# Kernel optimization log

Measured on AMD Instinct MI355X. Metric: run time of the kernel, lower is better.

Reference implementation:

```python
import jax, jax.numpy as jnp
import numpy as np

B, N, K = 32, 1024, 20

def _knn_idx(x, k):
    # x: [B, N, C] -> indices of k nearest neighbors (excluding self): [B, N, k]
    sq = jnp.sum(x * x, axis=-1)                      # [B, N]
    d = sq[:, :, None] + sq[:, None, :] - 2.0 * jnp.einsum('bnc,bmc->bnm', x, x)
    d = jnp.where(jnp.eye(x.shape[1], dtype=bool)[None], jnp.inf, d)
    _, idx = jax.lax.top_k(-d, k)                     # smallest distances
    return idx

def _edge_conv(x, k, mlp):
    # x: [B, N, C]; dynamic kNN graph + nn(cat[x_i, x_j - x_i]) + max over neighbors
    idx = _knn_idx(x, k)                              # [B, N, k]
    xj = jax.vmap(lambda xb, ib: xb[ib])(x, idx)      # [B, N, k, C]
    xi = jnp.broadcast_to(x[:, :, None, :], xj.shape)
    msg = mlp(jnp.concatenate([xi, xj - xi], axis=-1))  # [B, N, k, H]
    return jnp.max(msg, axis=2)                       # [B, N, H]

def setup_inputs() -> dict:
    key = jax.random.key(0)
    ks = jax.random.split(key, 16)
    def lin(kk, fi, fo):
        return jax.random.normal(kk, (fi, fo), dtype=jnp.float32) / np.sqrt(fi)
    x = jax.random.normal(ks[0], (B * N, 3), dtype=jnp.float32)
    batch = jnp.repeat(jnp.arange(B, dtype=jnp.int64), N)
    return {
        'x': x, 'batch': batch,
        'W1': lin(ks[1], 6, 64),   'b1': jnp.zeros((64,), jnp.float32),
        'W2': lin(ks[2], 64, 64),  'b2': jnp.zeros((64,), jnp.float32),
        'W3': lin(ks[3], 64, 64),  'b3': jnp.zeros((64,), jnp.float32),
        'W4': lin(ks[4], 128, 128),'b4': jnp.zeros((128,), jnp.float32),
        'Wp': lin(ks[5], 128, 512),'bp': jnp.zeros((512,), jnp.float32),
        'Wt1': lin(ks[6], 512, 256),'bt1': jnp.zeros((256,), jnp.float32),
        'Wt2': lin(ks[7], 256, 40), 'bt2': jnp.zeros((40,), jnp.float32),
    }

def reference(x, batch, W1, b1, W2, b2, W3, b3, W4, b4, Wp, bp, Wt1, bt1, Wt2, bt2):
    xb = x.reshape(B, N, -1)  # equal-sized clouds per batch vector
    mlp1 = lambda h: jax.nn.relu(jax.nn.relu(jax.nn.relu(h @ W1 + b1) @ W2 + b2) @ W3 + b3)
    mlp2 = lambda h: jax.nn.relu(h @ W4 + b4)
    out = _edge_conv(xb, K, mlp1)          # [B, N, 64]
    out = _edge_conv(out, K, mlp2)         # [B, N, 128]
    out = jax.nn.relu(out @ Wp + bp)       # [B, N, 512]
    out = jnp.max(out, axis=1)             # global max pool -> [B, 512]
    out = jax.nn.relu(out @ Wt1 + bt1) @ Wt2 + bt2  # [B, 40]
    return out
```

## Files before the change

### kernel.cpp

```cpp
#include <hip/hip_runtime.h>
#include <math.h>

#define BN   1024
#define NB   32
#define KNN  20
#define NROWS (NB*BN)

typedef __attribute__((ext_vector_type(8))) short bf16x8_t;
typedef __attribute__((ext_vector_type(4))) float f32x4_t;

__device__ __forceinline__ float finf() { return __builtin_huge_valf(); }

__device__ __forceinline__ unsigned short f2bf(float f) {
  union { float f; unsigned u; } v; v.f = f;
  unsigned r = v.u + 0x7FFFu + ((v.u >> 16) & 1u);
  return (unsigned short)(r >> 16);
}
__device__ __forceinline__ float bf2f(unsigned short h) {
  union { unsigned u; float f; } v; v.u = ((unsigned)h) << 16; return v.f;
}

__device__ __forceinline__ unsigned fkey(float d) {
  union { float f; unsigned u; } v; v.f = d;
  return (v.u & 0x80000000u) ? ~v.u : (v.u | 0x80000000u);
}

__device__ __forceinline__ void emit20(const unsigned (&kq)[16], unsigned thr,
                                       int lane, unsigned short* __restrict__ idx_out) {
  const unsigned long long lmask = (1ull << lane) - 1ull;
  int base = 0;
#pragma unroll
  for (int t = 0; t < 16; ++t) {
    const bool ok = (kq[t] <= thr);
    const unsigned long long m = __ballot(ok);
    if (ok) idx_out[base + (int)__popcll(m & lmask)] = (unsigned short)(kq[t] & 1023u);
    base += (int)__popcll(m);
  }
}

__device__ __forceinline__ void emit20c(const unsigned (&kq)[16], unsigned P, int cnt_lt,
                                        int lane, unsigned short* __restrict__ idx_out) {
  const unsigned long long lmask = (1ull << lane) - 1ull;
  const int need = KNN - cnt_lt;
  int base_lt = 0, base_eq = 0;
#pragma unroll
  for (int t = 0; t < 16; ++t) {
    const bool lt = (kq[t] < P);
    const bool eq = ((kq[t] - P) < 1024u);
    const unsigned long long mlt = __ballot(lt);
    const unsigned long long meq = __ballot(eq);
    if (lt) idx_out[base_lt + (int)__popcll(mlt & lmask)] = (unsigned short)(kq[t] & 1023u);
    const int erank = base_eq + (int)__popcll(meq & lmask);
    if (eq && erank < need) idx_out[cnt_lt + erank] = (unsigned short)(kq[t] & 1023u);
    base_lt += (int)__popcll(mlt);
    base_eq += (int)__popcll(meq);
  }
}

__device__ __forceinline__ void select20x2(const unsigned (&k0)[16], const unsigned (&k1)[16],
    int lane, unsigned short* __restrict__ o0, unsigned short* __restrict__ o1) {
  unsigned p0 = 0u, p1 = 0u;
  bool d0 = false, d1 = false;
#pragma unroll 1
  for (int b = 31; b >= 10; --b) {
    if (!d0) {
      const unsigned cand = p0 | (1u << b);
      int cnt = 0;
#pragma unroll
      for (int t = 0; t < 16; ++t) cnt += (int)__popcll(__ballot(k0[t] < cand));
      if (cnt == KNN)      { p0 = cand - 1u; d0 = true; }
      else if (cnt < KNN)  { p0 = cand; }
    }
    if (!d1) {
      const unsigned cand = p1 | (1u << b);
      int cnt = 0;
#pragma unroll
      for (int t = 0; t < 16; ++t) cnt += (int)__popcll(__ballot(k1[t] < cand));
      if (cnt == KNN)      { p1 = cand - 1u; d1 = true; }
      else if (cnt < KNN)  { p1 = cand; }
    }
    if (d0 && d1) break;
  }
  if (d0) emit20(k0, p0, lane, o0);
  else {
    int c = 0;
#pragma unroll
    for (int t = 0; t < 16; ++t) c += (int)__popcll(__ballot(k0[t] < p0));
    emit20c(k0, p0, c, lane, o0);
  }
  if (d1) emit20(k1, p1, lane, o1);
  else {
    int c = 0;
#pragma unroll
    for (int t = 0; t < 16; ++t) c += (int)__popcll(__ballot(k1[t] < p1));
    emit20c(k1, p1, c, lane, o1);
  }
}

__global__ __launch_bounds__(256) void prep_kernel(const float* __restrict__ W2, const float* __restrict__ W3,
    const float* __restrict__ W4, const float* __restrict__ Wp,
    unsigned short* __restrict__ w2b, unsigned short* __restrict__ w3b,
    unsigned short* __restrict__ w4b, unsigned short* __restrict__ wpb) {
  const int i = blockIdx.x * 256 + threadIdx.x;
  if (i < 512) {
    const int lane = i & 63, ks = (i >> 6) & 1, nt = i >> 7;
    const int col = nt*16 + (lane & 15), k0 = ks*32 + ((lane >> 4) << 3);
#pragma unroll
    for (int e = 0; e < 8; ++e) w2b[i*8 + e] = f2bf(W2[(size_t)(k0 + e)*64 + col]);
  } else if (i < 1024) {
    const int ii = i - 512;
    const int lane = ii & 63, ks = (ii >> 6) & 1, nt = ii >> 7;
    const int col = nt*16 + (lane & 15), k0 = ks*32 + ((lane >> 4) << 3);
#pragma unroll
    for (int e = 0; e < 8; ++e) w3b[ii*8 + e] = f2bf(W3[(size_t)(k0 + e)*64 + col]);
  } else if (i < 3072) {
    const int ii = i - 1024;
    const int lane = ii & 63, ks = (ii >> 6) & 3, nt = ii >> 8;
    const int col = nt*16 + (lane & 15), k0 = ks*32 + ((lane >> 4) << 3);
#pragma unroll
    for (int e = 0; e < 8; ++e) w4b[ii*8 + e] = f2bf(W4[(size_t)(k0 + e)*128 + col]);
  } else if (i < 11264) {
    const int ii = i - 3072;
    const int lane = ii & 63, ks = (ii >> 6) & 3, nt = ii >> 8;
    const int col = nt*16 + (lane & 15), k0 = ks*32 + ((lane >> 4) << 3);
#pragma unroll
    for (int e = 0; e < 8; ++e) {
      const float v = Wp[(size_t)(k0 + e)*512 + col];
      const unsigned short h = f2bf(v);
      wpb[ii*8 + e]         = h;
      wpb[65536 + ii*8 + e] = f2bf(v - bf2f(h));
    }
  }
}

__global__ __launch_bounds__(256) void knn3_kernel(const float* __restrict__ x, unsigned short* __restrict__ idxo) {
  const int pair = blockIdx.x * 4 + (threadIdx.x >> 6);
  const int lane = threadIdx.x & 63;
  const int row0 = pair * 2;
  const int b = row0 >> 10;
  const int ia = row0 & (BN - 1), ib = ia + 1;
  const float* xb = x + (size_t)b * BN * 3;
  const float xa0 = xb[ia*3+0], xa1 = xb[ia*3+1], xa2 = xb[ia*3+2];
  const float xb0 = xb[ib*3+0], xb1 = xb[ib*3+1], xb2 = xb[ib*3+2];
  const float sqa = xa0*xa0 + xa1*xa1 + xa2*xa2;
  const float sqb = xb0*xb0 + xb1*xb1 + xb2*xb2;
  unsigned k0[16], k1[16];
#pragma unroll
  for (int t = 0; t < 16; ++t) {
    const int j = (t << 6) | lane;
    const float a0 = xb[j*3+0], a1 = xb[j*3+1], a2 = xb[j*3+2];
    const float sqj = a0*a0 + a1*a1 + a2*a2;
    const float da  = sqa + sqj - 2.0f*(xa0*a0 + xa1*a1 + xa2*a2);
    const float db  = sqb + sqj - 2.0f*(xb0*a0 + xb1*a1 + xb2*a2);
    k0[t] = (j == ia) ? 0xFFFFFFFFu : ((fkey(da) & 0xFFFFFC00u) | (unsigned)j);
    k1[t] = (j == ib) ? 0xFFFFFFFFu : ((fkey(db) & 0xFFFFFC00u) | (unsigned)j);
  }
  select20x2(k0, k1, lane, idxo + (size_t)row0 * KNN, idxo + (size_t)(row0 + 1) * KNN);
}

__global__ __launch_bounds__(256) void edge1_mfma_kernel(const float* __restrict__ x, const unsigned short* __restrict__ idx,
    const float* __restrict__ W1, const float* __restrict__ B1,
    const unsigned short* __restrict__ w2b, const float* __restrict__ B2,
    const unsigned short* __restrict__ w3b, const float* __restrict__ B3,
    unsigned short* __restrict__ hib, unsigned short* __restrict__ lob,
    float* __restrict__ sqbuf) {
  __shared__ unsigned short Hs1[80*64];
  __shared__ unsigned short Hs2[80*64];
  __shared__ float part[4][4];
  const int t = threadIdx.x, lane = t & 63, w = t >> 6;
  const int node0 = blockIdx.x * 4;

  const int bcol = w*16 + (lane & 15);
  bf16x8_t Bf2[2], Bf3[2];
#pragma unroll
  for (int ks = 0; ks < 2; ++ks) {
    Bf2[ks] = *(const bf16x8_t*)&w2b[(size_t)((w*2 + ks)*64 + lane) * 8];
    Bf3[ks] = *(const bf16x8_t*)&w3b[(size_t)((w*2 + ks)*64 + lane) * 8];
  }

  float w1c[6];
#pragma unroll
  for (int c = 0; c < 6; ++c) w1c[c] = W1[c*64 + lane];
  const float b1o = B1[lane];
  for (int r = w; r < 80; r += 4) {
    const int g = (r * 205) >> 12;
    const int e = r - g*20;
    const int node = node0 + g;
    const int b = node >> 10;
    const int j = idx[(size_t)node*KNN + e];
    const float xi0 = x[(size_t)node*3+0], xi1 = x[(size_t)node*3+1], xi2 = x[(size_t)node*3+2];
    const size_t jr = ((size_t)(b*BN + j))*3;
    const float h3 = x[jr+0]-xi0, h4 = x[jr+1]-xi1, h5 = x[jr+2]-xi2;
    float z = b1o + xi0*w1c[0] + xi1*w1c[1] + xi2*w1c[2]
                  + h3*w1c[3] + h4*w1c[4] + h5*w1c[5];
    z = fmaxf(z, 0.0f);
    Hs1[r*64 + (((lane>>3) ^ (r&7))<<3) + (lane&7)] = f2bf(z);
  }
  __syncthreads();

  f32x4_t acc[5];
#pragma unroll
  for (int mt = 0; mt < 5; ++mt) acc[mt] = (f32x4_t){0,0,0,0};
#pragma unroll
  for (int ks = 0; ks < 2; ++ks) {
#pragma unroll
    for (int mt = 0; mt < 5; ++mt) {
      const int r = mt*16 + (lane & 15);
      const int chunk = ks*4 + (lane >> 4);
      const bf16x8_t a = *(const bf16x8_t*)&Hs1[r*64 + ((chunk ^ (r&7))<<3)];
      acc[mt] = __builtin_amdgcn_mfma_f32_16x16x32_bf16(a, Bf2[ks], acc[mt], 0,0,0);
    }
  }
  {
    const float b2o = B2[bcol];
    const int rbase = (lane >> 4) * 4;
#pragma unroll
    for (int mt = 0; mt < 5; ++mt) {
#pragma unroll
      for (int reg = 0; reg < 4; ++reg) {
        const int row = mt*16 + rbase + reg;
        const float v = fmaxf(acc[mt][reg] + b2o, 0.0f);
        Hs2[row*64 + (((bcol>>3) ^ (row&7))<<3) + (bcol&7)] = f2bf(v);
      }
    }
  }
  __syncthreads();

#pragma unroll
  for (int mt = 0; mt < 5; ++mt) acc[mt] = (f32x4_t){0,0,0,0};
#pragma unroll
  for (int ks = 0; ks < 2; ++ks) {
#pragma unroll
    for (int mt = 0; mt < 5; ++mt) {
      const int r = mt*16 + (lane & 15);
      const int chunk = ks*4 + (lane >> 4);
      const bf16x8_t a = *(const bf16x8_t*)&Hs2[r*64 + ((chunk ^ (r&7))<<3)];
      acc[mt] = __builtin_amdgcn_mfma_f32_16x16x32_bf16(a, Bf3[ks], acc[mt], 0,0,0);
    }
  }

  {
    const float b3o = B3[bcol];
    const int rbase = (lane >> 4) * 4;
    float nm0 = 0.0f, nm1 = 0.0f, nm2 = 0.0f, nm3 = 0.0f;
#pragma unroll
    for (int mt = 0; mt < 5; ++mt) {
#pragma unroll
      for (int reg = 0; reg < 4; ++reg) {
        const int r = mt*16 + rbase + reg;
        const int g = (r * 205) >> 12;
        const float v = fmaxf(acc[mt][reg] + b3o, 0.0f);
        nm0 = (g == 0) ? fmaxf(nm0, v) : nm0;
        nm1 = (g == 1) ? fmaxf(nm1, v) : nm1;
        nm2 = (g == 2) ? fmaxf(nm2, v) : nm2;
        nm3 = (g == 3) ? fmaxf(nm3, v) : nm3;
      }
    }
#pragma unroll
    for (int off = 16; off <= 32; off <<= 1) {
      nm0 = fmaxf(nm0, __shfl_xor(nm0, off, 64));
      nm1 = fmaxf(nm1, __shfl_xor(nm1, off, 64));
      nm2 = fmaxf(nm2, __shfl_xor(nm2, off, 64));
      nm3 = fmaxf(nm3, __shfl_xor(nm3, off, 64));
    }
    const int gq = lane >> 4;
    const float m = (gq == 0) ? nm0 : (gq == 1) ? nm1 : (gq == 2) ? nm2 : nm3;
    const int node = node0 + gq;
    const unsigned short h = f2bf(m);
    hib[(size_t)node*64 + bcol] = h;
    lob[(size_t)node*64 + bcol] = f2bf(m - bf2f(h));
    float s = m * m;
#pragma unroll
    for (int off = 1; off <= 8; off <<= 1) s += __shfl_xor(s, off, 64);
    if ((lane & 15) == 0) part[gq][w] = s;
  }
  __syncthreads();
  if (t < 4) sqbuf[node0 + t] = part[t][0] + part[t][1] + part[t][2] + part[t][3];
}

__global__ __launch_bounds__(512) void knn64edge2_kernel(
    const unsigned short* __restrict__ hi, const unsigned short* __restrict__ lo,
    const float* __restrict__ sq, const unsigned short* __restrict__ w4b,
    const float* __restrict__ B4,
    unsigned short* __restrict__ o2hi, unsigned short* __restrict__ o2lo) {
  __shared__ unsigned Dmat[16 * 1024];
  __shared__ unsigned short idx_sh[16][KNN];
  unsigned short* Hs = (unsigned short*)Dmat;
  const int t = threadIdx.x, lane = t & 63, w = t >> 6;
  const int i0  = blockIdx.x * 16;
  const int b   = i0 >> 10;
  const int i0l = i0 & (BN - 1);

  {
    const size_t arow = (size_t)(i0 + (lane & 15)) * 64;
    const int    koff = (lane >> 4) * 8;
    bf16x8_t Ahi[2], Alo[2];
#pragma unroll
    for (int ks = 0; ks < 2; ++ks) {
      Ahi[ks] = *(const bf16x8_t*)&hi[arow + ks*32 + koff];
      Alo[ks] = *(const bf16x8_t*)&lo[arow + ks*32 + koff];
    }
    f32x4_t acc[8];
#pragma unroll
    for (int nt = 0; nt < 8; ++nt) {
      const int jl = (8*w + nt)*16 + (lane & 15);
      const size_t jrow = ((size_t)(b << 10) + jl) * 64;
      const bf16x8_t Bhi0 = *(const bf16x8_t*)&hi[jrow + koff];
      const bf16x8_t Bhi1 = *(const bf16x8_t*)&hi[jrow + 32 + koff];
      const bf16x8_t Blo0 = *(const bf16x8_t*)&lo[jrow + koff];
      const bf16x8_t Blo1 = *(const bf16x8_t*)&lo[jrow + 32 + koff];
      f32x4_t a = (f32x4_t){0,0,0,0};
      a = __builtin_amdgcn_mfma_f32_16x16x32_bf16(Ahi[0], Bhi0, a, 0,0,0);
      a = __builtin_amdgcn_mfma_f32_16x16x32_bf16(Ahi[1], Bhi1, a, 0,0,0);
      a = __builtin_amdgcn_mfma_f32_16x16x32_bf16(Ahi[0], Blo0, a, 0,0,0);
      a = __builtin_amdgcn_mfma_f32_16x16x32_bf16(Ahi[1], Blo1, a, 0,0,0);
      a = __builtin_amdgcn_mfma_f32_16x16x32_bf16(Alo[0], Bhi0, a, 0,0,0);
      a = __builtin_amdgcn_mfma_f32_16x16x32_bf16(Alo[1], Bhi1, a, 0,0,0);
      acc[nt] = a;
    }
    const int rbase = (lane >> 4) * 4;
    float sqr[4];
#pragma unroll
    for (int r = 0; r < 4; ++r) sqr[r] = sq[i0 + rbase + r];
#pragma unroll
    for (int nt = 0; nt < 8; ++nt) {
      const int jl = (8*w + nt)*16 + (lane & 15);
      const float sqj = sq[(b << 10) + jl];
#pragma unroll
      for (int r = 0; r < 4; ++r) {
        const float d = sqr[r] + sqj - 2.0f * acc[nt][r];
        const unsigned kq = (jl == i0l + rbase + r) ? 0xFFFFFFFFu
                          : ((fkey(d) & 0xFFFFFC00u) | (unsigned)jl);
        Dmat[(rbase + r)*1024 + jl] = kq;
      }
    }
  }
  __syncthreads();

  {
    const int r0 = 2*w, r1 = 2*w + 1;
    unsigned k0[16], k1[16];
#pragma unroll
    for (int tt = 0; tt < 16; ++tt) {
      k0[tt] = Dmat[r0*1024 + tt*64 + lane];
      k1[tt] = Dmat[r1*1024 + tt*64 + lane];
    }
    select20x2(k0, k1, lane, &idx_sh[r0][0], &idx_sh[r1][0]);
  }
  __syncthreads();

  bf16x8_t Bfrag[4];
#pragma unroll
  for (int ks = 0; ks < 4; ++ks)
    Bfrag[ks] = *(const bf16x8_t*)&w4b[(size_t)((w*4 + ks)*64 + lane) * 8];
  const float bb = B4[w*16 + (lane & 15)];
  const int cq = (lane & 15) * 4;
  const int ch1 = cq >> 3, ch2 = 8 + (cq >> 3), sub = cq & 4;
  const int rbase = (lane >> 4) * 4;

#pragma unroll 1
  for (int h = 0; h < 2; ++h) {
    const int mynode = i0 + h*8 + w;
    const size_t noff = (size_t)mynode*64 + cq;
    const ushort4 hxi = *(const ushort4*)&hi[noff];
    const ushort4 lxi = *(const ushort4*)&lo[noff];
    const float xi0 = bf2f(hxi.x) + bf2f(lxi.x);
    const float xi1 = bf2f(hxi.y) + bf2f(lxi.y);
    const float xi2 = bf2f(hxi.z) + bf2f(lxi.z);
    const float xi3 = bf2f(hxi.w) + bf2f(lxi.w);
#pragma unroll
    for (int i = 0; i < 5; ++i) {
      const int e = i*4 + (lane >> 4);
      const int j = idx_sh[h*8 + w][e];
      const size_t joff = ((size_t)(b*BN + j))*64 + cq;
      const ushort4 hxj = *(const ushort4*)&hi[joff];
      const ushort4 lxj = *(const ushort4*)&lo[joff];
      ushort4 hdf;
      hdf.x = f2bf(bf2f(hxj.x) + bf2f(lxj.x) - xi0);
      hdf.y = f2bf(bf2f(hxj.y) + bf2f(lxj.y) - xi1);
      hdf.z = f2bf(bf2f(hxj.z) + bf2f(lxj.z) - xi2);
      hdf.w = f2bf(bf2f(hxj.w) + bf2f(lxj.w) - xi3);
      const int r = w*20 + e;
      *(ushort4*)&Hs[r*128 + ((ch1 ^ (r&7))<<3) + sub] = hxi;
      *(ushort4*)&Hs[r*128 + ((ch2 ^ (r&7))<<3) + sub] = hdf;
    }
    __syncthreads();

    f32x4_t acc2[10];
#pragma unroll
    for (int mt = 0; mt < 10; ++mt) acc2[mt] = (f32x4_t){0,0,0,0};
#pragma unroll
    for (int ks = 0; ks < 4; ++ks) {
#pragma unroll
      for (int mt = 0; mt < 10; ++mt) {
        const int r = mt*16 + (lane & 15);
        const int chunk = ks*4 + (lane >> 4);
        const bf16x8_t a = *(const bf16x8_t*)&Hs[r*128 + ((chunk ^ (r&7))<<3)];
        acc2[mt] = __builtin_amdgcn_mfma_f32_16x16x32_bf16(a, Bfrag[ks], acc2[mt], 0,0,0);
      }
    }

    float nm[8];
#pragma unroll
    for (int g = 0; g < 8; ++g) nm[g] = 0.0f;
#pragma unroll
    for (int mt = 0; mt < 10; ++mt) {
#pragma unroll
      for (int reg = 0; reg < 4; ++reg) {
        const int base = mt*16 + reg;
        const int glo = base / 20, ghi = (base + 12) / 20;
        const int r = base + rbase;
        const float v = fmaxf(acc2[mt][reg] + bb, 0.0f);
        if (glo == ghi) {
          nm[glo] = fmaxf(nm[glo], v);
        } else {
          const bool hi2 = (r >= ghi*20);
          nm[glo] = hi2 ? nm[glo] : fmaxf(nm[glo], v);
          nm[ghi] = hi2 ? fmaxf(nm[ghi], v) : nm[ghi];
        }
      }
    }
#pragma unroll
    for (int off = 16; off <= 32; off <<= 1)
#pragma unroll
      for (int g = 0; g < 8; ++g) nm[g] = fmaxf(nm[g], __shfl_xor(nm[g], off, 64));
    const int gq = lane >> 4;
#pragma unroll
    for (int g = 0; g < 8; ++g) {
      if ((g & 3) == gq) {
        const float m = nm[g];
        const size_t o = (size_t)(i0 + h*8 + g)*128 + w*16 + (lane & 15);
        const unsigned short hh = f2bf(m);
        o2hi[o] = hh;
        o2lo[o] = f2bf(m - bf2f(hh));
      }
    }
    __syncthreads();
  }
}

__global__ __launch_bounds__(512) void pool_mfma_kernel(const unsigned short* __restrict__ o2hi,
    const unsigned short* __restrict__ o2lo, const unsigned short* __restrict__ wpb,
    const float* __restrict__ bp, float* __restrict__ pooled) {
  const int t = threadIdx.x, lane = t & 63, w = t >> 6;
  const int b = blockIdx.x >> 3, chunk = blockIdx.x & 7;
  const int row0 = b*BN + chunk*128;
  const int koff = (lane >> 4) * 8;
  bf16x8_t Bhi[4][4], Blo[4][4];
#pragma unroll
  for (int q = 0; q < 4; ++q)
#pragma unroll
    for (int ks = 0; ks < 4; ++ks) {
      const int nt = w*4 + q;
      Bhi[q][ks] = *(const bf16x8_t*)&wpb[(size_t)((nt*4 + ks)*64 + lane) * 8];
      Blo[q][ks] = *(const bf16x8_t*)&wpb[65536 + (size_t)((nt*4 + ks)*64 + lane) * 8];
    }
  float colmax[4] = {-finf(), -finf(), -finf(), -finf()};
#pragma unroll 2
  for (int mt = 0; mt < 8; ++mt) {
    const size_t ar = (size_t)(row0 + mt*16 + (lane & 15)) * 128;
    bf16x8_t Ahi[4], Alo[4];
#pragma unroll
    for (int ks = 0; ks < 4; ++ks) {
      Ahi[ks] = *(const bf16x8_t*)&o2hi[ar + ks*32 + koff];
      Alo[ks] = *(const bf16x8_t*)&o2lo[ar + ks*32 + koff];
    }
#pragma unroll
    for (int q = 0; q < 4; ++q) {
      f32x4_t a = (f32x4_t){0,0,0,0};
#pragma unroll
      for (int ks = 0; ks < 4; ++ks) {
        a = __builtin_amdgcn_mfma_f32_16x16x32_bf16(Ahi[ks], Bhi[q][ks], a, 0,0,0);
        a = __builtin_amdgcn_mfma_f32_16x16x32_bf16(Ahi[ks], Blo[q][ks], a, 0,0,0);
        a = __builtin_amdgcn_mfma_f32_16x16x32_bf16(Alo[ks], Bhi[q][ks], a, 0,0,0);
      }
#pragma unroll
      for (int reg = 0; reg < 4; ++reg) colmax[q] = fmaxf(colmax[q], a[reg]);
    }
  }
#pragma unroll
  for (int off = 16; off <= 32; off <<= 1)
#pragma unroll
    for (int q = 0; q < 4; ++q) colmax[q] = fmaxf(colmax[q], __shfl_xor(colmax[q], off, 64));
  if (lane < 16) {
#pragma unroll
    for (int q = 0; q < 4; ++q) {
      const int col = (w*4 + q)*16 + lane;
      const float m = fmaxf(colmax[q] + bp[col], 0.0f);
      atomicMax((int*)(pooled + (size_t)b*512 + col), __float_as_int(m));
    }
  }
}

__global__ __launch_bounds__(256) void head_kernel(const float* __restrict__ pooled,
    const float* __restrict__ Wt1, const float* __restrict__ bt1,
    const float* __restrict__ Wt2, const float* __restrict__ bt2,
    float* __restrict__ out) {
  __shared__ float psh[512];
  __shared__ float h1sh[256];
  const int t = threadIdx.x, b = blockIdx.x;
  psh[t]       = pooled[(size_t)b*512 + t];
  psh[t + 256] = pooled[(size_t)b*512 + t + 256];
  __syncthreads();
  float z = bt1[t];
  for (int j = 0; j < 512; ++j) z += psh[j] * Wt1[(size_t)j*256 + t];
  h1sh[t] = fmaxf(z, 0.0f);
  __syncthreads();
  if (t < 40) {
    float z2 = bt2[t];
    for (int j = 0; j < 256; ++j) z2 += h1sh[j] * Wt2[(size_t)j*40 + t];
    out[(size_t)b*40 + t] = z2;
  }
}

extern "C" void kernel_launch(void* const* d_in, const int* in_sizes, int n_in,
                              void* d_out, int out_size, void* d_ws, size_t ws_size,
                              hipStream_t stream) {
  const float* x   = (const float*)d_in[0];
  const float* W1  = (const float*)d_in[2];
  const float* B1  = (const float*)d_in[3];
  const float* W2  = (const float*)d_in[4];
  const float* B2  = (const float*)d_in[5];
  const float* W3  = (const float*)d_in[6];
  const float* B3  = (const float*)d_in[7];
  const float* W4  = (const float*)d_in[8];
  const float* B4  = (const float*)d_in[9];
  const float* Wp  = (const float*)d_in[10];
  const float* bp  = (const float*)d_in[11];
  const float* Wt1 = (const float*)d_in[12];
  const float* bt1 = (const float*)d_in[13];
  const float* Wt2 = (const float*)d_in[14];
  const float* bt2 = (const float*)d_in[15];
  float* out = (float*)d_out;

  char* ws = (char*)d_ws;
  const size_t OFF_SQ     = 0;
  const size_t OFF_IDX1   = 131072;
  const size_t OFF_HIB    = 1441792;
  const size_t OFF_LOB    = 5636096;
  const size_t OFF_O2HI   = 9830400;
  const size_t OFF_O2LO   = 18219008;
  const size_t OFF_POOLED = 26607616;
  const size_t OFF_W2B    = 26673152;
  const size_t OFF_W3B    = 26681344;
  const size_t OFF_W4B    = 26689536;
  const size_t OFF_WPB    = 26722304;
  const size_t WS_NEEDED  = 26984448;
  if (ws_size < WS_NEEDED) return;

  float*          sqbuf  = (float*)(ws + OFF_SQ);
  unsigned short* idx1   = (unsigned short*)(ws + OFF_IDX1);
  unsigned short* hib    = (unsigned short*)(ws + OFF_HIB);
  unsigned short* lob    = (unsigned short*)(ws + OFF_LOB);
  unsigned short* o2hi   = (unsigned short*)(ws + OFF_O2HI);
  unsigned short* o2lo   = (unsigned short*)(ws + OFF_O2LO);
  float*          pooled = (float*)(ws + OFF_POOLED);
  unsigned short* w2b    = (unsigned short*)(ws + OFF_W2B);
  unsigned short* w3b    = (unsigned short*)(ws + OFF_W3B);
  unsigned short* w4b    = (unsigned short*)(ws + OFF_W4B);
  unsigned short* wpb    = (unsigned short*)(ws + OFF_WPB);

  prep_kernel       <<<44,          256, 0, stream>>>(W2, W3, W4, Wp, w2b, w3b, w4b, wpb);
  knn3_kernel       <<<NROWS/8,     256, 0, stream>>>(x, idx1);
  edge1_mfma_kernel <<<NROWS/4,     256, 0, stream>>>(x, idx1, W1, B1, w2b, B2, w3b, B3,
                                                      hib, lob, sqbuf);
  knn64edge2_kernel <<<NROWS/16,    512, 0, stream>>>(hib, lob, sqbuf, w4b, B4, o2hi, o2lo);
  hipMemsetAsync(pooled, 0, NB*512*sizeof(float), stream);
  pool_mfma_kernel  <<<NB*8,        512, 0, stream>>>(o2hi, o2lo, wpb, bp, pooled);
  head_kernel       <<<NB,          256, 0, stream>>>(pooled, Wt1, bt1, Wt2, bt2, out);
}
```

Measured before the change: 332.6 us.

## Fuse 3D kNN selection into first edge-conv kernel with 8 nodes per block

Merges the xyz kNN kernel into the first EdgeConv MFMA kernel. Each block now computes neighbor indices for 8 nodes into shared memory and then runs the 3-layer MLP and neighbor max on 160 edge rows. This removes one kernel launch and the global round trip of the index buffer, and doubles the rows per MFMA tile. The cost is more shared memory and accumulator registers per block, which may lower occupancy, plus more complex group-max bookkeeping.

```diff
diff --git a/kernel.cpp b/kernel.cpp
--- a/kernel.cpp
+++ b/kernel.cpp
@@ -133,61 +133,52 @@
   }
 }
 
-__global__ __launch_bounds__(256) void knn3_kernel(const float* __restrict__ x, unsigned short* __restrict__ idxo) {
-  const int pair = blockIdx.x * 4 + (threadIdx.x >> 6);
-  const int lane = threadIdx.x & 63;
-  const int row0 = pair * 2;
-  const int b = row0 >> 10;
-  const int ia = row0 & (BN - 1), ib = ia + 1;
-  const float* xb = x + (size_t)b * BN * 3;
-  const float xa0 = xb[ia*3+0], xa1 = xb[ia*3+1], xa2 = xb[ia*3+2];
-  const float xb0 = xb[ib*3+0], xb1 = xb[ib*3+1], xb2 = xb[ib*3+2];
-  const float sqa = xa0*xa0 + xa1*xa1 + xa2*xa2;
-  const float sqb = xb0*xb0 + xb1*xb1 + xb2*xb2;
-  unsigned k0[16], k1[16];
-#pragma unroll
-  for (int t = 0; t < 16; ++t) {
-    const int j = (t << 6) | lane;
-    const float a0 = xb[j*3+0], a1 = xb[j*3+1], a2 = xb[j*3+2];
-    const float sqj = a0*a0 + a1*a1 + a2*a2;
-    const float da  = sqa + sqj - 2.0f*(xa0*a0 + xa1*a1 + xa2*a2);
-    const float db  = sqb + sqj - 2.0f*(xb0*a0 + xb1*a1 + xb2*a2);
-    k0[t] = (j == ia) ? 0xFFFFFFFFu : ((fkey(da) & 0xFFFFFC00u) | (unsigned)j);
-    k1[t] = (j == ib) ? 0xFFFFFFFFu : ((fkey(db) & 0xFFFFFC00u) | (unsigned)j);
-  }
-  select20x2(k0, k1, lane, idxo + (size_t)row0 * KNN, idxo + (size_t)(row0 + 1) * KNN);
-}
-
-__global__ __launch_bounds__(256) void edge1_mfma_kernel(const float* __restrict__ x, const unsigned short* __restrict__ idx,
+__global__ __launch_bounds__(256) void knn3edge1_kernel(const float* __restrict__ x,
     const float* __restrict__ W1, const float* __restrict__ B1,
     const unsigned short* __restrict__ w2b, const float* __restrict__ B2,
     const unsigned short* __restrict__ w3b, const float* __restrict__ B3,
     unsigned short* __restrict__ hib, unsigned short* __restrict__ lob,
     float* __restrict__ sqbuf) {
-  __shared__ unsigned short Hs1[80*64];
-  __shared__ unsigned short Hs2[80*64];
-  __shared__ float part[4][4];
+  __shared__ unsigned short Hs1[160*64];
+  __shared__ unsigned short Hs2[160*64];
+  __shared__ unsigned short idx_sh[8][KNN];
+  __shared__ float part[8][4];
   const int t = threadIdx.x, lane = t & 63, w = t >> 6;
-  const int node0 = blockIdx.x * 4;
-
-  const int bcol = w*16 + (lane & 15);
-  bf16x8_t Bf2[2], Bf3[2];
-#pragma unroll
-  for (int ks = 0; ks < 2; ++ks) {
-    Bf2[ks] = *(const bf16x8_t*)&w2b[(size_t)((w*2 + ks)*64 + lane) * 8];
-    Bf3[ks] = *(const bf16x8_t*)&w3b[(size_t)((w*2 + ks)*64 + lane) * 8];
-  }
+  const int i0  = blockIdx.x * 8;
+  const int b   = i0 >> 10;
+  const int i0l = i0 & (BN - 1);
+  const float* xb = x + (size_t)b * BN * 3;
+
+  {
+    const int ia = i0l + 2*w, ib = ia + 1;
+    const float xa0 = xb[ia*3+0], xa1 = xb[ia*3+1], xa2 = xb[ia*3+2];
+    const float xb0 = xb[ib*3+0], xb1 = xb[ib*3+1], xb2 = xb[ib*3+2];
+    const float sqa = xa0*xa0 + xa1*xa1 + xa2*xa2;
+    const float sqb = xb0*xb0 + xb1*xb1 + xb2*xb2;
+    unsigned k0[16], k1[16];
+#pragma unroll
+    for (int tt = 0; tt < 16; ++tt) {
+      const int j = (tt << 6) | lane;
+      const float a0 = xb[j*3+0], a1 = xb[j*3+1], a2 = xb[j*3+2];
+      const float sqj = a0*a0 + a1*a1 + a2*a2;
+      const float da  = sqa + sqj - 2.0f*(xa0*a0 + xa1*a1 + xa2*a2);
+      const float db  = sqb + sqj - 2.0f*(xb0*a0 + xb1*a1 + xb2*a2);
+      k0[tt] = (j == ia) ? 0xFFFFFFFFu : ((fkey(da) & 0xFFFFFC00u) | (unsigned)j);
+      k1[tt] = (j == ib) ? 0xFFFFFFFFu : ((fkey(db) & 0xFFFFFC00u) | (unsigned)j);
+    }
+    select20x2(k0, k1, lane, &idx_sh[2*w][0], &idx_sh[2*w + 1][0]);
+  }
+  __syncthreads();
 
   float w1c[6];
 #pragma unroll
   for (int c = 0; c < 6; ++c) w1c[c] = W1[c*64 + lane];
   const float b1o = B1[lane];
-  for (int r = w; r < 80; r += 4) {
+  for (int r = w; r < 160; r += 4) {
     const int g = (r * 205) >> 12;
     const int e = r - g*20;
-    const int node = node0 + g;
-    const int b = node >> 10;
-    const int j = idx[(size_t)node*KNN + e];
+    const int node = i0 + g;
+    const int j = idx_sh[g][e];
     const float xi0 = x[(size_t)node*3+0], xi1 = x[(size_t)node*3+1], xi2 = x[(size_t)node*3+2];
     const size_t jr = ((size_t)(b*BN + j))*3;
     const float h3 = x[jr+0]-xi0, h4 = x[jr+1]-xi1, h5 = x[jr+2]-xi2;
@@ -198,13 +189,20 @@
   }
   __syncthreads();
 
-  f32x4_t acc[5];
-#pragma unroll
-  for (int mt = 0; mt < 5; ++mt) acc[mt] = (f32x4_t){0,0,0,0};
+  const int bcol = w*16 + (lane & 15);
+  bf16x8_t Bf2[2], Bf3[2];
 #pragma unroll
   for (int ks = 0; ks < 2; ++ks) {
-#pragma unroll
-    for (int mt = 0; mt < 5; ++mt) {
+    Bf2[ks] = *(const bf16x8_t*)&w2b[(size_t)((w*2 + ks)*64 + lane) * 8];
+    Bf3[ks] = *(const bf16x8_t*)&w3b[(size_t)((w*2 + ks)*64 + lane) * 8];
+  }
+  f32x4_t acc[10];
+#pragma unroll
+  for (int mt = 0; mt < 10; ++mt) acc[mt] = (f32x4_t){0,0,0,0};
+#pragma unroll
+  for (int ks = 0; ks < 2; ++ks) {
+#pragma unroll
+    for (int mt = 0; mt < 10; ++mt) {
       const int r = mt*16 + (lane & 15);
       const int chunk = ks*4 + (lane >> 4);
       const bf16x8_t a = *(const bf16x8_t*)&Hs1[r*64 + ((chunk ^ (r&7))<<3)];
@@ -215,7 +213,7 @@
     const float b2o = B2[bcol];
     const int rbase = (lane >> 4) * 4;
 #pragma unroll
-    for (int mt = 0; mt < 5; ++mt) {
+    for (int mt = 0; mt < 10; ++mt) {
 #pragma unroll
       for (int reg = 0; reg < 4; ++reg) {
         const int row = mt*16 + rbase + reg;
@@ -227,11 +225,11 @@
   __syncthreads();
 
 #pragma unroll
-  for (int mt = 0; mt < 5; ++mt) acc[mt] = (f32x4_t){0,0,0,0};
+  for (int mt = 0; mt < 10; ++mt) acc[mt] = (f32x4_t){0,0,0,0};
 #pragma unroll
   for (int ks = 0; ks < 2; ++ks) {
 #pragma unroll
-    for (int mt = 0; mt < 5; ++mt) {
+    for (int mt = 0; mt < 10; ++mt) {
       const int r = mt*16 + (lane & 15);
       const int chunk = ks*4 + (lane >> 4);
       const bf16x8_t a = *(const bf16x8_t*)&Hs2[r*64 + ((chunk ^ (r&7))<<3)];
@@ -242,40 +240,48 @@
   {
     const float b3o = B3[bcol];
     const int rbase = (lane >> 4) * 4;
-    float nm0 = 0.0f, nm1 = 0.0f, nm2 = 0.0f, nm3 = 0.0f;
-#pragma unroll
-    for (int mt = 0; mt < 5; ++mt) {
+    float nm[8];
+#pragma unroll
+    for (int g = 0; g < 8; ++g) nm[g] = 0.0f;
+#pragma unroll
+    for (int mt = 0; mt < 10; ++mt) {
 #pragma unroll
       for (int reg = 0; reg < 4; ++reg) {
-        const int r = mt*16 + rbase + reg;
-        const int g = (r * 205) >> 12;
+        const int base = mt*16 + reg;
+        const int glo = base / 20, ghi = (base + 12) / 20;
+        const int r = base + rbase;
         const float v = fmaxf(acc[mt][reg] + b3o, 0.0f);
-        nm0 = (g == 0) ? fmaxf(nm0, v) : nm0;
-        nm1 = (g == 1) ? fmaxf(nm1, v) : nm1;
-        nm2 = (g == 2) ? fmaxf(nm2, v) : nm2;
-        nm3 = (g == 3) ? fmaxf(nm3, v) : nm3;
-      }
-    }
-#pragma unroll
-    for (int off = 16; off <= 32; off <<= 1) {
-      nm0 = fmaxf(nm0, __shfl_xor(nm0, off, 64));
-      nm1 = fmaxf(nm1, __shfl_xor(nm1, off, 64));
-      nm2 = fmaxf(nm2, __shfl_xor(nm2, off, 64));
-      nm3 = fmaxf(nm3, __shfl_xor(nm3, off, 64));
-    }
+        if (glo == ghi) {
+          nm[glo] = fmaxf(nm[glo], v);
+        } else {
+          const bool hi2 = (r >= ghi*20);
+          nm[glo] = hi2 ? nm[glo] : fmaxf(nm[glo], v);
+          nm[ghi] = hi2 ? fmaxf(nm[ghi], v) : nm[ghi];
+        }
+      }
+    }
+#pragma unroll
+    for (int off = 16; off <= 32; off <<= 1)
+#pragma unroll
+      for (int g = 0; g < 8; ++g) nm[g] = fmaxf(nm[g], __shfl_xor(nm[g], off, 64));
     const int gq = lane >> 4;
-    const float m = (gq == 0) ? nm0 : (gq == 1) ? nm1 : (gq == 2) ? nm2 : nm3;
-    const int node = node0 + gq;
-    const unsigned short h = f2bf(m);
-    hib[(size_t)node*64 + bcol] = h;
-    lob[(size_t)node*64 + bcol] = f2bf(m - bf2f(h));
-    float s = m * m;
-#pragma unroll
-    for (int off = 1; off <= 8; off <<= 1) s += __shfl_xor(s, off, 64);
-    if ((lane & 15) == 0) part[gq][w] = s;
-  }
-  __syncthreads();
-  if (t < 4) sqbuf[node0 + t] = part[t][0] + part[t][1] + part[t][2] + part[t][3];
+#pragma unroll
+    for (int g = 0; g < 8; ++g) {
+      if ((g & 3) == gq) {
+        const float m = nm[g];
+        const size_t o = (size_t)(i0 + g)*64 + w*16 + (lane & 15);
+        const unsigned short h = f2bf(m);
+        hib[o] = h;
+        lob[o] = f2bf(m - bf2f(h));
+        float s = m * m;
+#pragma unroll
+        for (int off = 1; off <= 8; off <<= 1) s += __shfl_xor(s, off, 64);
+        if ((lane & 15) == 0) part[g][w] = s;
+      }
+    }
+  }
+  __syncthreads();
+  if (t < 8) sqbuf[i0 + t] = part[t][0] + part[t][1] + part[t][2] + part[t][3];
 }
 
 __global__ __launch_bounds__(512) void knn64edge2_kernel(
@@ -535,7 +541,6 @@
 
   char* ws = (char*)d_ws;
   const size_t OFF_SQ     = 0;
-  const size_t OFF_IDX1   = 131072;
   const size_t OFF_HIB    = 1441792;
   const size_t OFF_LOB    = 5636096;
   const size_t OFF_O2HI   = 9830400;
@@ -549,7 +554,6 @@
   if (ws_size < WS_NEEDED) return;
 
   float*          sqbuf  = (float*)(ws + OFF_SQ);
-  unsigned short* idx1   = (unsigned short*)(ws + OFF_IDX1);
   unsigned short* hib    = (unsigned short*)(ws + OFF_HIB);
   unsigned short* lob    = (unsigned short*)(ws + OFF_LOB);
   unsigned short* o2hi   = (unsigned short*)(ws + OFF_O2HI);
@@ -561,8 +565,7 @@
   unsigned short* wpb    = (unsigned short*)(ws + OFF_WPB);
 
   prep_kernel       <<<44,          256, 0, stream>>>(W2, W3, W4, Wp, w2b, w3b, w4b, wpb);
-  knn3_kernel       <<<NROWS/8,     256, 0, stream>>>(x, idx1);
-  edge1_mfma_kernel <<<NROWS/4,     256, 0, stream>>>(x, idx1, W1, B1, w2b, B2, w3b, B3,
+  knn3edge1_kernel  <<<NROWS/8,     256, 0, stream>>>(x, W1, B1, w2b, B2, w3b, B3,
                                                       hib, lob, sqbuf);
   knn64edge2_kernel <<<NROWS/16,    512, 0, stream>>>(hib, lob, sqbuf, w4b, B4, o2hi, o2lo);
   hipMemsetAsync(pooled, 0, NB*512*sizeof(float), stream);
```

After: 391.0 us. +17.6%, slower.
